# Performance work log

Hardware: AMD Instinct MI355X
Metric: run time of the kernel (lower is better)

## Reference

```python
import jax, jax.numpy as jnp
import numpy as np

N_NODES = 100_000
N_EDGES = 800_000
D = 96
BN_EPS = 1e-5
LEAKY_SLOPE = 0.01


def setup_inputs() -> dict:
    key = jax.random.key(0)
    ks = jax.random.split(key, 9)
    x = jax.random.normal(ks[0], (N_NODES, D), dtype=jnp.float32)
    edge_index = jax.random.randint(ks[1], (2, N_EDGES), 0, N_NODES, dtype=jnp.int64)
    s = 0.05
    return {
        "x": x,
        "edge_index": edge_index,
        # SAGEConv #1 (mean aggregator, bias=False)
        "W_self1": jax.random.normal(ks[2], (D, D), dtype=jnp.float32) * s,
        "W_neigh1": jax.random.normal(ks[3], (D, D), dtype=jnp.float32) * s,
        # SAGEConv #2 (pool aggregator): fc_pool has bias, fc_self/fc_neigh bias=False
        "W_pool": jax.random.normal(ks[4], (D, D), dtype=jnp.float32) * s,
        "b_pool": jax.random.normal(ks[5], (D,), dtype=jnp.float32) * s,
        "W_self2": jax.random.normal(ks[6], (D, D), dtype=jnp.float32) * s,
        "W_neigh2": jax.random.normal(ks[7], (D, D), dtype=jnp.float32) * s,
        # BatchNorm affine params
        "g1": jnp.ones((D,), jnp.float32),
        "beta1": jnp.zeros((D,), jnp.float32),
        "g2": jnp.ones((D,), jnp.float32),
        "beta2": jnp.zeros((D,), jnp.float32),
    }


def _batch_norm(h, gamma, beta):
    # training-mode BatchNorm1d: biased batch stats over nodes
    mu = h.mean(axis=0)
    var = jnp.mean(jnp.square(h - mu), axis=0)
    return gamma * (h - mu) * jax.lax.rsqrt(var + BN_EPS) + beta


def _forward(x, edge_index, W_self1, W_neigh1, W_pool, b_pool, W_self2, W_neigh2,
             g1, beta1, g2, beta2):
    src, dst = edge_index[0], edge_index[1]
    n = x.shape[0]
    deg = jax.ops.segment_sum(jnp.ones((src.shape[0],), x.dtype), dst, num_segments=n)

    # ---- SAGEConv (mean): h_neigh = mean_{u in N(v)} x_u ; out = x W_self + h_neigh W_neigh
    agg_sum = jax.ops.segment_sum(x[src], dst, num_segments=n)          # [N, D]
    h_mean = agg_sum / jnp.maximum(deg, 1.0)[:, None]                   # 0 for isolated nodes
    out1 = x @ W_self1 + h_mean @ W_neigh1
    out1 = _batch_norm(out1, g1, beta1)

    # ---- SAGEConv (pool): h_neigh = max_{u in N(v)} relu(x_u W_pool + b_pool)
    hp = jax.nn.relu(x @ W_pool + b_pool)                               # [N, D]
    agg_max = jax.ops.segment_max(hp[src], dst, num_segments=n)        # -inf where empty
    h_max = jnp.where(deg[:, None] > 0, agg_max, 0.0)
    out2 = x @ W_self2 + h_max @ W_neigh2
    out2 = _batch_norm(out2, g2, beta2)

    return jax.nn.leaky_relu(out1 + out2, negative_slope=LEAKY_SLOPE)


def reference(x, edge_index, W_self1, W_neigh1, W_pool, b_pool, W_self2, W_neigh2,
              g1, beta1, g2, beta2):
    return _forward(x, edge_index, W_self1, W_neigh1, W_pool, b_pool,
                    W_self2, W_neigh2, g1, beta1, g2, beta2)
```

## Files before the change

kernel.cpp:

```cpp
#include <hip/hip_runtime.h>

#define NN 100000
#define NE 800000
#define DD 96
#define NROWPAD 100096
#define GBLK 782
#define DBLK 391
#define SCAN_BLOCKS 100
#define SCAN_CHUNK 1000

typedef __attribute__((ext_vector_type(8))) short bf16x8;
typedef __attribute__((ext_vector_type(4))) float f32x4;
typedef unsigned short u16;
typedef unsigned int u32;

#define MFMA16 __builtin_amdgcn_mfma_f32_16x16x32_bf16

#define OFF_DEG      0u
#define OFF_ROWSTART 100000u
#define OFF_CURSOR   200004u
#define OFF_BSUM     300004u
#define OFF_STATS    300132u
#define OFF_PARAMS   300516u
#define OFF_WT       300900u
#define OFF_CSR      323940u
#define OFF_XH       1123940u
#define OFF_HMBF     10733156u
#define OFF_HXBF     15537764u

__device__ __forceinline__ u16 f2b(float f) {
  u32 u = __float_as_uint(f);
  u += 0x7FFFu + ((u >> 16) & 1u);
  return (u16)(u >> 16);
}
__device__ __forceinline__ float b2f(short h) {
  return __uint_as_float(((u32)(u16)h) << 16);
}

__global__ void wprep_kernel(const float* __restrict__ Ws1, const float* __restrict__ Wn1,
                             const float* __restrict__ Ws2, const float* __restrict__ Wn2,
                             const float* __restrict__ Wp, u16* __restrict__ wt) {
  int idx = blockIdx.x * 256 + threadIdx.x;
  if (idx >= 5 * 9216) return;
  int m = idx / 9216, r = idx % 9216;
  int k = r / 96, c = r % 96;
  const float* W = (m == 0) ? Ws1 : (m == 1) ? Wn1 : (m == 2) ? Ws2 : (m == 3) ? Wn2 : Wp;
  wt[m * 9216 + c * 96 + k] = f2b(W[k * 96 + c]);
}

__global__ void deg_kernel(const int* __restrict__ dst, int* __restrict__ deg) {
  int e = blockIdx.x * blockDim.x + threadIdx.x;
  if (e >= NE) return;
  atomicAdd(&deg[dst[e]], 1);
}

__global__ void scan_sum_kernel(const int* __restrict__ deg, int* __restrict__ bsum) {
  __shared__ int red[256];
  int t = threadIdx.x;
  int base = blockIdx.x * SCAN_CHUNK;
  int s = 0;
  for (int i = t; i < SCAN_CHUNK; i += 256) s += deg[base + i];
  red[t] = s;
  __syncthreads();
  for (int off = 128; off > 0; off >>= 1) {
    if (t < off) red[t] += red[t + off];
    __syncthreads();
  }
  if (t == 0) bsum[blockIdx.x] = red[0];
}

__global__ void scan_bsum_kernel(int* __restrict__ bsum, int* __restrict__ row_start) {
  __shared__ int sm[128];
  int t = threadIdx.x;
  int v = (t < SCAN_BLOCKS) ? bsum[t] : 0;
  sm[t] = v;
  __syncthreads();
  for (int off = 1; off < 128; off <<= 1) {
    int u = 0;
    if (t >= off) u = sm[t - off];
    __syncthreads();
    if (t >= off) sm[t] += u;
    __syncthreads();
  }
  if (t < SCAN_BLOCKS) bsum[t] = sm[t] - v;
  if (t == SCAN_BLOCKS - 1) row_start[NN] = sm[t];
}

__global__ void scan_final_kernel(const int* __restrict__ deg,
                                  const int* __restrict__ bsum,
                                  int* __restrict__ row_start,
                                  int* __restrict__ cursor) {
  __shared__ int sm[256];
  int t = threadIdx.x;
  int base = blockIdx.x * SCAN_CHUNK + t * 4;
  int4 d = {0, 0, 0, 0};
  if (t < 250) d = *reinterpret_cast<const int4*>(deg + base);
  int tot = d.x + d.y + d.z + d.w;
  sm[t] = tot;
  __syncthreads();
  for (int off = 1; off < 256; off <<= 1) {
    int u = 0;
    if (t >= off) u = sm[t - off];
    __syncthreads();
    if (t >= off) sm[t] += u;
    __syncthreads();
  }
  if (t < 250) {
    int run = bsum[blockIdx.x] + sm[t] - tot;
    int4 rs;
    rs.x = run;
    rs.y = run + d.x;
    rs.z = run + d.x + d.y;
    rs.w = run + d.x + d.y + d.z;
    *reinterpret_cast<int4*>(row_start + base) = rs;
    *reinterpret_cast<int4*>(cursor + base) = rs;
  }
}

__global__ void fill_csr_kernel(const int* __restrict__ src,
                                const int* __restrict__ dst,
                                int* __restrict__ cursor,
                                int* __restrict__ csr) {
  int e = blockIdx.x * blockDim.x + threadIdx.x;
  if (e >= NE) return;
  int pos = atomicAdd(&cursor[dst[e]], 1);
  csr[pos] = src[e];
}

__global__ __launch_bounds__(512) void hp_gemm_kernel(const float* __restrict__ x,
                                                      const u16* __restrict__ wt,
                                                      const float* __restrict__ bp,
                                                      u16* __restrict__ xh) {
  __shared__ bf16x8 wl[1152];
  int t = threadIdx.x;
  const bf16x8* wg = reinterpret_cast<const bf16x8*>(wt + 4 * 9216);
  for (int j = t; j < 1152; j += 512) wl[j] = wg[j];
  __syncthreads();
  int w = t >> 6, lane = t & 63;
  int i = lane & 15, g = lane >> 4;
  int row_base = blockIdx.x * 128 + w * 16;
  int grow_a = row_base + i;
  int lrow = grow_a < NN ? grow_a : NN - 1;
  const float4* xr = reinterpret_cast<const float4*>(x + (size_t)lrow * 96);
  bf16x8* xhv = reinterpret_cast<bf16x8*>(xh);
  bf16x8 ax[3];
#pragma unroll
  for (int kb = 0; kb < 3; ++kb) {
    float4 p = xr[(kb * 4 + g) * 2];
    float4 q = xr[(kb * 4 + g) * 2 + 1];
    bf16x8 v;
    v[0] = (short)f2b(p.x); v[1] = (short)f2b(p.y); v[2] = (short)f2b(p.z); v[3] = (short)f2b(p.w);
    v[4] = (short)f2b(q.x); v[5] = (short)f2b(q.y); v[6] = (short)f2b(q.z); v[7] = (short)f2b(q.w);
    ax[kb] = v;
    xhv[(size_t)grow_a * 24 + kb * 4 + g] = v;
  }
  for (int nt = 0; nt < 6; ++nt) {
    f32x4 acc = {0.f, 0.f, 0.f, 0.f};
    int bch = (nt * 16 + i) * 12;
#pragma unroll
    for (int kb = 0; kb < 3; ++kb)
      acc = MFMA16(ax[kb], wl[bch + kb * 4 + g], acc, 0, 0, 0);
    int col = nt * 16 + i;
    float bias = bp[col];
#pragma unroll
    for (int r = 0; r < 4; ++r) {
      int grow = row_base + g * 4 + r;
      xh[(size_t)grow * 192 + 96 + col] = f2b(fmaxf(acc[r] + bias, 0.0f));
    }
  }
}

__global__ __launch_bounds__(384) void gather_kernel(const u16* __restrict__ xh,
                                                     const int* __restrict__ row_start,
                                                     const int* __restrict__ csr,
                                                     u16* __restrict__ hmbf,
                                                     u16* __restrict__ hxbf) {
  int t = threadIdx.x;
  int node = blockIdx.x * 32 + (t & 31);
  int slot = t >> 5;
  bool isMax = slot >= 6;
  if (node >= NN) return;
  int beg = row_start[node], end = row_start[node + 1];
  int cbase = slot * 2;
  const bf16x8* XH = reinterpret_cast<const bf16x8*>(xh);
  float a0[8], a1[8];
#pragma unroll
  for (int j = 0; j < 8; ++j) { a0[j] = 0.f; a1[j] = 0.f; }
  int e = beg;
  for (; e + 4 <= end; e += 4) {
    size_t b0 = (size_t)csr[e] * 24 + cbase;
    size_t b1 = (size_t)csr[e + 1] * 24 + cbase;
    size_t b2 = (size_t)csr[e + 2] * 24 + cbase;
    size_t b3 = (size_t)csr[e + 3] * 24 + cbase;
    bf16x8 u0 = XH[b0], v0 = XH[b0 + 1];
    bf16x8 u1 = XH[b1], v1 = XH[b1 + 1];
    bf16x8 u2 = XH[b2], v2 = XH[b2 + 1];
    bf16x8 u3 = XH[b3], v3 = XH[b3 + 1];
    if (isMax) {
#pragma unroll
      for (int j = 0; j < 8; ++j) {
        a0[j] = fmaxf(a0[j], fmaxf(fmaxf(b2f(u0[j]), b2f(u1[j])), fmaxf(b2f(u2[j]), b2f(u3[j]))));
        a1[j] = fmaxf(a1[j], fmaxf(fmaxf(b2f(v0[j]), b2f(v1[j])), fmaxf(b2f(v2[j]), b2f(v3[j]))));
      }
    } else {
#pragma unroll
      for (int j = 0; j < 8; ++j) {
        a0[j] += (b2f(u0[j]) + b2f(u1[j])) + (b2f(u2[j]) + b2f(u3[j]));
        a1[j] += (b2f(v0[j]) + b2f(v1[j])) + (b2f(v2[j]) + b2f(v3[j]));
      }
    }
  }
  for (; e < end; ++e) {
    size_t b0 = (size_t)csr[e] * 24 + cbase;
    bf16x8 u0 = XH[b0], v0 = XH[b0 + 1];
    if (isMax) {
#pragma unroll
      for (int j = 0; j < 8; ++j) {
        a0[j] = fmaxf(a0[j], b2f(u0[j]));
        a1[j] = fmaxf(a1[j], b2f(v0[j]));
      }
    } else {
#pragma unroll
      for (int j = 0; j < 8; ++j) {
        a0[j] += b2f(u0[j]);
        a1[j] += b2f(v0[j]);
      }
    }
  }
  float scl = isMax ? 1.0f : ((end > beg) ? 1.0f / (float)(end - beg) : 0.0f);
  bf16x8 w0, w1;
#pragma unroll
  for (int j = 0; j < 8; ++j) {
    w0[j] = (short)f2b(a0[j] * scl);
    w1[j] = (short)f2b(a1[j] * scl);
  }
  u16* dstp = isMax ? hxbf : hmbf;
  int outc = isMax ? (slot - 6) * 2 : slot * 2;
  bf16x8* dv = reinterpret_cast<bf16x8*>(dstp);
  size_t ob = (size_t)node * 12 + outc;
  dv[ob] = w0; dv[ob + 1] = w1;
}

__global__ __launch_bounds__(1024) void dualgemm_kernel(const u16* __restrict__ xh,
                                                        u16* __restrict__ hmbf,
                                                        u16* __restrict__ hxbf,
                                                        const u16* __restrict__ wt,
                                                        float* __restrict__ stats) {
  __shared__ bf16x8 wl[4608];
  __shared__ float smst[384];
  int t = threadIdx.x;
  const bf16x8* wg = reinterpret_cast<const bf16x8*>(wt);
  for (int j = t; j < 4608; j += 1024) wl[j] = wg[j];
  for (int j = t; j < 384; j += 1024) smst[j] = 0.f;
  __syncthreads();
  int w = t >> 6, lane = t & 63;
  int i = lane & 15, g = lane >> 4;
  int row_base = blockIdx.x * 256 + w * 16;
  size_t arowx = (size_t)(row_base + i) * 24;
  size_t arowh = (size_t)(row_base + i) * 12;
  bf16x8 ax[3], am[3], ah[3];
#pragma unroll
  for (int kb = 0; kb < 3; ++kb) {
    ax[kb] = reinterpret_cast<const bf16x8*>(xh)[arowx + kb * 4 + g];
    am[kb] = reinterpret_cast<const bf16x8*>(hmbf)[arowh + kb * 4 + g];
    ah[kb] = reinterpret_cast<const bf16x8*>(hxbf)[arowh + kb * 4 + g];
  }
  __syncthreads();
  for (int nt = 0; nt < 6; ++nt) {
    f32x4 a1 = {0.f, 0.f, 0.f, 0.f}, a2 = {0.f, 0.f, 0.f, 0.f};
    int bch = (nt * 16 + i) * 12;
#pragma unroll
    for (int kb = 0; kb < 3; ++kb) {
      int bc = bch + kb * 4 + g;
      a1 = MFMA16(ax[kb], wl[bc], a1, 0, 0, 0);
      a1 = MFMA16(am[kb], wl[1152 + bc], a1, 0, 0, 0);
      a2 = MFMA16(ax[kb], wl[2304 + bc], a2, 0, 0, 0);
      a2 = MFMA16(ah[kb], wl[3456 + bc], a2, 0, 0, 0);
    }
    int col = nt * 16 + i;
    float s1 = 0, q1 = 0, s2 = 0, q2 = 0;
#pragma unroll
    for (int r = 0; r < 4; ++r) {
      int grow = row_base + g * 4 + r;
      if (grow < NN) {
        float v = a1[r], u = a2[r];
        s1 += v; q1 += v * v; s2 += u; q2 += u * u;
        hmbf[(size_t)grow * 96 + col] = f2b(v);
        hxbf[(size_t)grow * 96 + col] = f2b(u);
      }
    }
    s1 += __shfl_xor(s1, 16); q1 += __shfl_xor(q1, 16);
    s2 += __shfl_xor(s2, 16); q2 += __shfl_xor(q2, 16);
    s1 += __shfl_xor(s1, 32); q1 += __shfl_xor(q1, 32);
    s2 += __shfl_xor(s2, 32); q2 += __shfl_xor(q2, 32);
    if (g == 0) {
      atomicAdd(&smst[col], s1);
      atomicAdd(&smst[96 + col], q1);
      atomicAdd(&smst[192 + col], s2);
      atomicAdd(&smst[288 + col], q2);
    }
  }
  __syncthreads();
  for (int j = t; j < 384; j += 1024) atomicAdd(&stats[j], smst[j]);
}

__global__ void finalize_kernel(const float* __restrict__ stats,
                                const float* __restrict__ g1, const float* __restrict__ beta1,
                                const float* __restrict__ g2, const float* __restrict__ beta2,
                                float* __restrict__ params) {
  int c = threadIdx.x;
  if (c >= 96) return;
  const float inv_n = 1.0f / NN;
  float mu1 = stats[c] * inv_n;
  float var1 = fmaxf(stats[96 + c] * inv_n - mu1 * mu1, 0.0f);
  float is1 = rsqrtf(var1 + 1e-5f);
  float a1 = g1[c] * is1;
  params[c] = a1;
  params[96 + c] = beta1[c] - a1 * mu1;
  float mu2 = stats[192 + c] * inv_n;
  float var2 = fmaxf(stats[288 + c] * inv_n - mu2 * mu2, 0.0f);
  float is2 = rsqrtf(var2 + 1e-5f);
  float a2 = g2[c] * is2;
  params[192 + c] = a2;
  params[288 + c] = beta2[c] - a2 * mu2;
}

__global__ __launch_bounds__(256) void final_kernel(const u16* __restrict__ o1,
                                                    const u16* __restrict__ o2,
                                                    const float* __restrict__ params,
                                                    float* __restrict__ out) {
  int idx = blockIdx.x * 256 + threadIdx.x;
  if (idx >= NN * 12) return;
  int c8 = idx % 12;
  bf16x8 v1 = reinterpret_cast<const bf16x8*>(o1)[idx];
  bf16x8 v2 = reinterpret_cast<const bf16x8*>(o2)[idx];
  const float4* P = reinterpret_cast<const float4*>(params);
  float4 A1l = P[c8 * 2],      A1h = P[c8 * 2 + 1];
  float4 B1l = P[24 + c8 * 2], B1h = P[24 + c8 * 2 + 1];
  float4 A2l = P[48 + c8 * 2], A2h = P[48 + c8 * 2 + 1];
  float4 B2l = P[72 + c8 * 2], B2h = P[72 + c8 * 2 + 1];
  float A1[8] = {A1l.x, A1l.y, A1l.z, A1l.w, A1h.x, A1h.y, A1h.z, A1h.w};
  float B1[8] = {B1l.x, B1l.y, B1l.z, B1l.w, B1h.x, B1h.y, B1h.z, B1h.w};
  float A2[8] = {A2l.x, A2l.y, A2l.z, A2l.w, A2h.x, A2h.y, A2h.z, A2h.w};
  float B2[8] = {B2l.x, B2l.y, B2l.z, B2l.w, B2h.x, B2h.y, B2h.z, B2h.w};
  float o[8];
#pragma unroll
  for (int j = 0; j < 8; ++j) {
    float v = A1[j] * b2f(v1[j]) + B1[j] + A2[j] * b2f(v2[j]) + B2[j];
    o[j] = v > 0.f ? v : 0.01f * v;
  }
  float4* ov = reinterpret_cast<float4*>(out);
  float4 lo = {o[0], o[1], o[2], o[3]}, hi = {o[4], o[5], o[6], o[7]};
  ov[idx * 2] = lo;
  ov[idx * 2 + 1] = hi;
}

extern "C" void kernel_launch(void* const* d_in, const int* in_sizes, int n_in,
                              void* d_out, int out_size, void* d_ws, size_t ws_size,
                              hipStream_t stream) {
  const float* x       = (const float*)d_in[0];
  const int*   ei      = (const int*)d_in[1];
  const float* W_self1 = (const float*)d_in[2];
  const float* W_neigh1= (const float*)d_in[3];
  const float* W_pool  = (const float*)d_in[4];
  const float* b_pool  = (const float*)d_in[5];
  const float* W_self2 = (const float*)d_in[6];
  const float* W_neigh2= (const float*)d_in[7];
  const float* g1      = (const float*)d_in[8];
  const float* beta1   = (const float*)d_in[9];
  const float* g2      = (const float*)d_in[10];
  const float* beta2   = (const float*)d_in[11];
  float* out = (float*)d_out;

  float* ws = (float*)d_ws;
  int*   deg       = (int*)(ws + OFF_DEG);
  int*   row_start = (int*)(ws + OFF_ROWSTART);
  int*   cursor    = (int*)(ws + OFF_CURSOR);
  int*   bsum      = (int*)(ws + OFF_BSUM);
  float* stats     = ws + OFF_STATS;
  float* params    = ws + OFF_PARAMS;
  u16*   wt        = (u16*)(ws + OFF_WT);
  int*   csr       = (int*)(ws + OFF_CSR);
  u16*   xh        = (u16*)(ws + OFF_XH);
  u16*   hmbf      = (u16*)(ws + OFF_HMBF);
  u16*   hxbf      = (u16*)(ws + OFF_HXBF);

  const int* src = ei;
  const int* dst = ei + NE;

  hipMemsetAsync(deg, 0, NN * sizeof(int), stream);
  hipMemsetAsync(stats, 0, 384 * sizeof(float), stream);

  wprep_kernel<<<(5 * 9216 + 255) / 256, 256, 0, stream>>>(W_self1, W_neigh1, W_self2,
                                                           W_neigh2, W_pool, wt);

  deg_kernel<<<(NE + 255) / 256, 256, 0, stream>>>(dst, deg);
  scan_sum_kernel<<<SCAN_BLOCKS, 256, 0, stream>>>(deg, bsum);
  scan_bsum_kernel<<<1, 128, 0, stream>>>(bsum, row_start);
  scan_final_kernel<<<SCAN_BLOCKS, 256, 0, stream>>>(deg, bsum, row_start, cursor);
  fill_csr_kernel<<<(NE + 255) / 256, 256, 0, stream>>>(src, dst, cursor, csr);

  hp_gemm_kernel<<<GBLK, 512, 0, stream>>>(x, wt, b_pool, xh);

  gather_kernel<<<(NN + 31) / 32, 384, 0, stream>>>(xh, row_start, csr, hmbf, hxbf);

  dualgemm_kernel<<<DBLK, 1024, 0, stream>>>(xh, hmbf, hxbf, wt, stats);
  finalize_kernel<<<1, 128, 0, stream>>>(stats, g1, beta1, g2, beta2, params);
  final_kernel<<<(NN * 12 + 255) / 256, 256, 0, stream>>>(hmbf, hxbf, params, out);
}
```

Measured before the change: 274.2 us.

## Restructure neighbor gather: wider per-thread chunks, index prefetch, integer bf16 max

The gather kernel now uses 8 thread slots per node, each loading 3 bf16x8 vectors (48 bytes) per neighbor instead of 12 slots with 2 vectors, which cuts the thread count and repeated index loads. Neighbor indices are software-prefetched one iteration ahead with a 2-edge unroll instead of the previous 4-edge unroll. The max-pool path compares raw bf16 bit patterns as unsigned integers, which is valid because the values are non-negative after ReLU, and skips float conversion. This lowers instruction count and index traffic, at the cost of less memory-level parallelism per thread from the smaller unroll.

New measurement: 261.0 us. -4.8%, faster.

```diff
diff --git a/kernel.cpp b/kernel.cpp
--- a/kernel.cpp
+++ b/kernel.cpp
@@ -10,6 +10,7 @@
 #define SCAN_CHUNK 1000
 
 typedef __attribute__((ext_vector_type(8))) short bf16x8;
+typedef __attribute__((ext_vector_type(8))) unsigned short u16x8;
 typedef __attribute__((ext_vector_type(4))) float f32x4;
 typedef unsigned short u16;
 typedef unsigned int u32;
@@ -170,7 +171,7 @@
   }
 }
 
-__global__ __launch_bounds__(384) void gather_kernel(const u16* __restrict__ xh,
+__global__ __launch_bounds__(256) void gather_kernel(const u16* __restrict__ xh,
                                                      const int* __restrict__ row_start,
                                                      const int* __restrict__ csr,
                                                      u16* __restrict__ hmbf,
@@ -178,67 +179,82 @@
   int t = threadIdx.x;
   int node = blockIdx.x * 32 + (t & 31);
   int slot = t >> 5;
-  bool isMax = slot >= 6;
+  bool isMax = slot >= 4;
   if (node >= NN) return;
   int beg = row_start[node], end = row_start[node + 1];
-  int cbase = slot * 2;
-  const bf16x8* XH = reinterpret_cast<const bf16x8*>(xh);
-  float a0[8], a1[8];
-#pragma unroll
-  for (int j = 0; j < 8; ++j) { a0[j] = 0.f; a1[j] = 0.f; }
+  int cbase = slot * 3;
+  const u16x8* XH = reinterpret_cast<const u16x8*>(xh);
+  float s0[8], s1[8], s2[8];
+  u16x8 m0, m1, m2;
+#pragma unroll
+  for (int j = 0; j < 8; ++j) {
+    s0[j] = 0.f; s1[j] = 0.f; s2[j] = 0.f;
+    m0[j] = 0; m1[j] = 0; m2[j] = 0;
+  }
   int e = beg;
-  for (; e + 4 <= end; e += 4) {
-    size_t b0 = (size_t)csr[e] * 24 + cbase;
-    size_t b1 = (size_t)csr[e + 1] * 24 + cbase;
-    size_t b2 = (size_t)csr[e + 2] * 24 + cbase;
-    size_t b3 = (size_t)csr[e + 3] * 24 + cbase;
-    bf16x8 u0 = XH[b0], v0 = XH[b0 + 1];
-    bf16x8 u1 = XH[b1], v1 = XH[b1 + 1];
-    bf16x8 u2 = XH[b2], v2 = XH[b2 + 1];
-    bf16x8 u3 = XH[b3], v3 = XH[b3 + 1];
+  int i0 = csr[(e < end) ? e : 0];
+  int i1 = csr[(e + 1 < end) ? e + 1 : ((end > beg) ? end - 1 : 0)];
+  for (; e + 2 <= end; e += 2) {
+    int p2 = e + 2, p3 = e + 3;
+    int n0 = csr[(p2 < end) ? p2 : end - 1];
+    int n1 = csr[(p3 < end) ? p3 : end - 1];
+    size_t b0 = (size_t)i0 * 24 + cbase;
+    size_t b1 = (size_t)i1 * 24 + cbase;
+    u16x8 u0 = XH[b0], u1 = XH[b0 + 1], u2 = XH[b0 + 2];
+    u16x8 v0 = XH[b1], v1 = XH[b1 + 1], v2 = XH[b1 + 2];
     if (isMax) {
 #pragma unroll
       for (int j = 0; j < 8; ++j) {
-        a0[j] = fmaxf(a0[j], fmaxf(fmaxf(b2f(u0[j]), b2f(u1[j])), fmaxf(b2f(u2[j]), b2f(u3[j]))));
-        a1[j] = fmaxf(a1[j], fmaxf(fmaxf(b2f(v0[j]), b2f(v1[j])), fmaxf(b2f(v2[j]), b2f(v3[j]))));
+        u16 a = u0[j] > v0[j] ? u0[j] : v0[j]; m0[j] = m0[j] > a ? m0[j] : a;
+        u16 b = u1[j] > v1[j] ? u1[j] : v1[j]; m1[j] = m1[j] > b ? m1[j] : b;
+        u16 c = u2[j] > v2[j] ? u2[j] : v2[j]; m2[j] = m2[j] > c ? m2[j] : c;
       }
     } else {
 #pragma unroll
       for (int j = 0; j < 8; ++j) {
-        a0[j] += (b2f(u0[j]) + b2f(u1[j])) + (b2f(u2[j]) + b2f(u3[j]));
-        a1[j] += (b2f(v0[j]) + b2f(v1[j])) + (b2f(v2[j]) + b2f(v3[j]));
+        s0[j] += b2f((short)u0[j]) + b2f((short)v0[j]);
+        s1[j] += b2f((short)u1[j]) + b2f((short)v1[j]);
+        s2[j] += b2f((short)u2[j]) + b2f((short)v2[j]);
       }
     }
-  }
-  for (; e < end; ++e) {
-    size_t b0 = (size_t)csr[e] * 24 + cbase;
-    bf16x8 u0 = XH[b0], v0 = XH[b0 + 1];
+    i0 = n0; i1 = n1;
+  }
+  if (e < end) {
+    size_t b0 = (size_t)i0 * 24 + cbase;
+    u16x8 u0 = XH[b0], u1 = XH[b0 + 1], u2 = XH[b0 + 2];
     if (isMax) {
 #pragma unroll
       for (int j = 0; j < 8; ++j) {
-        a0[j] = fmaxf(a0[j], b2f(u0[j]));
-        a1[j] = fmaxf(a1[j], b2f(v0[j]));
+        m0[j] = m0[j] > u0[j] ? m0[j] : u0[j];
+        m1[j] = m1[j] > u1[j] ? m1[j] : u1[j];
+        m2[j] = m2[j] > u2[j] ? m2[j] : u2[j];
       }
     } else {
 #pragma unroll
       for (int j = 0; j < 8; ++j) {
-        a0[j] += b2f(u0[j]);
-        a1[j] += b2f(v0[j]);
+        s0[j] += b2f((short)u0[j]);
+        s1[j] += b2f((short)u1[j]);
+        s2[j] += b2f((short)u2[j]);
       }
     }
   }
-  float scl = isMax ? 1.0f : ((end > beg) ? 1.0f / (float)(end - beg) : 0.0f);
-  bf16x8 w0, w1;
-#pragma unroll
-  for (int j = 0; j < 8; ++j) {
-    w0[j] = (short)f2b(a0[j] * scl);
-    w1[j] = (short)f2b(a1[j] * scl);
-  }
-  u16* dstp = isMax ? hxbf : hmbf;
-  int outc = isMax ? (slot - 6) * 2 : slot * 2;
-  bf16x8* dv = reinterpret_cast<bf16x8*>(dstp);
-  size_t ob = (size_t)node * 12 + outc;
-  dv[ob] = w0; dv[ob + 1] = w1;
+  if (isMax) {
+    u16x8* dv = reinterpret_cast<u16x8*>(hxbf);
+    size_t ob = (size_t)node * 12 + (slot - 4) * 3;
+    dv[ob] = m0; dv[ob + 1] = m1; dv[ob + 2] = m2;
+  } else {
+    float scl = (end > beg) ? 1.0f / (float)(end - beg) : 0.0f;
+    u16x8 w0, w1, w2;
+#pragma unroll
+    for (int j = 0; j < 8; ++j) {
+      w0[j] = f2b(s0[j] * scl);
+      w1[j] = f2b(s1[j] * scl);
+      w2[j] = f2b(s2[j] * scl);
+    }
+    u16x8* dv = reinterpret_cast<u16x8*>(hmbf);
+    size_t ob = (size_t)node * 12 + slot * 3;
+    dv[ob] = w0; dv[ob + 1] = w1; dv[ob + 2] = w2;
+  }
 }
 
 __global__ __launch_bounds__(1024) void dualgemm_kernel(const u16* __restrict__ xh,
@@ -402,7 +418,7 @@
 
   hp_gemm_kernel<<<GBLK, 512, 0, stream>>>(x, wt, b_pool, xh);
 
-  gather_kernel<<<(NN + 31) / 32, 384, 0, stream>>>(xh, row_start, csr, hmbf, hxbf);
+  gather_kernel<<<(NN + 31) / 32, 256, 0, stream>>>(xh, row_start, csr, hmbf, hxbf);
 
   dualgemm_kernel<<<DBLK, 1024, 0, stream>>>(xh, hmbf, hxbf, wt, stats);
   finalize_kernel<<<1, 128, 0, stream>>>(stats, g1, beta1, g2, beta2, params);
```
